# Kernel optimization log

Hardware: AMD Instinct MI355X
Metric: run time of the kernel (lower is better)

## Reference

```python
import jax, jax.numpy as jnp
import numpy as np

N_NODES = 100000
KERNEL_SIZE = 2  # per dim, dim=1 -> 2 kernel weight matrices


def spline_conv(x, edge_index, W, root, bias):
    """PyG SplineConv, dim=1, kernel_size=2, degree=1 open B-spline, aggr='mean'.

    edge_attr is ones (built inside the torch forward), clamped to [0,1].
    Open linear B-spline with K=2: v = u*(K-1); idx = clip(floor(v), 0, K-2) == 0;
    frac = v - idx. Basis weights (1-frac, frac) on kernel indices (0, 1).
    """
    src, dst = edge_index[0], edge_index[1]  # messages flow src -> dst
    E = src.shape[0]
    u = jnp.ones((E,), x.dtype)              # edge pseudo-coordinates (clamped ones)
    v = u * (KERNEL_SIZE - 1)
    idx = jnp.clip(jnp.floor(v), 0, KERNEL_SIZE - 2)  # always 0 for K=2
    frac = v - idx                            # in [0,1]
    # Transform all nodes by both kernel weight matrices once: (2, N, out)
    xw = jnp.einsum('ni,kio->kno', x, W)
    # Per-edge basis-weighted message (idx==0 => kernel indices 0 and 1)
    msg = (1.0 - frac)[:, None] * xw[0, src] + frac[:, None] * xw[1, src]
    agg = jax.ops.segment_sum(msg, dst, num_segments=N_NODES)
    deg = jax.ops.segment_sum(jnp.ones((E,), x.dtype), dst, num_segments=N_NODES)
    agg = agg / jnp.clip(deg, 1.0)[:, None]   # mean aggregation
    return agg + x @ root + bias


def setup_inputs() -> dict:
    key = jax.random.key(0)
    ks = jax.random.split(key, 8)
    N, F, H, C, E = N_NODES, 128, 16, 40, 3200000
    x = jax.random.normal(ks[0], (N, F), dtype=jnp.float32)
    edge_index = jax.random.randint(ks[1], (2, E), 0, N, dtype=jnp.int32)
    W1 = jax.random.normal(ks[2], (2, F, H), dtype=jnp.float32) * 0.1
    root1 = jax.random.normal(ks[3], (F, H), dtype=jnp.float32) * 0.1
    b1 = jnp.zeros((H,), dtype=jnp.float32)
    W2 = jax.random.normal(ks[4], (2, H, C), dtype=jnp.float32) * 0.1
    root2 = jax.random.normal(ks[5], (H, C), dtype=jnp.float32) * 0.1
    b2 = jnp.zeros((C,), dtype=jnp.float32)
    return {"x": x, "edge_index": edge_index, "W1": W1, "root1": root1,
            "b1": b1, "W2": W2, "root2": root2, "b2": b2}


def reference(x, edge_index, W1, root1, b1, W2, root2, b2):
    # eval mode: F.dropout(training=False) is identity
    h = jax.nn.elu(spline_conv(x, edge_index, W1, root1, b1))
    out = spline_conv(h, edge_index, W2, root2, b2)
    return jax.nn.log_softmax(out, axis=1)
```

## Files before the change

### kernel.cpp

```cpp
#include <hip/hip_runtime.h>
#include <hip/hip_bf16.h>

#define N_NODES 100000
#define FIN 128
#define HID 16
#define NCLS 40
#define NEDGE 3200000
#define NBUCK 391
#define NCHUNK 782
#define W_ROW 144

typedef int v4i __attribute__((ext_vector_type(4)));

__device__ __forceinline__ unsigned short f2b(float f) {
  union { float f; unsigned u; } v;
  v.f = f;
  unsigned r = v.u + 0x7FFFu + ((v.u >> 16) & 1u);
  return (unsigned short)(r >> 16);
}

__device__ __forceinline__ void accum8(uint4 w, float* a) {
  union { unsigned u; float f; } t;
  t.u = w.x << 16;         a[0] += t.f;
  t.u = w.x & 0xFFFF0000u; a[1] += t.f;
  t.u = w.y << 16;         a[2] += t.f;
  t.u = w.y & 0xFFFF0000u; a[3] += t.f;
  t.u = w.z << 16;         a[4] += t.f;
  t.u = w.z & 0xFFFF0000u; a[5] += t.f;
  t.u = w.w << 16;         a[6] += t.f;
  t.u = w.w & 0xFFFF0000u; a[7] += t.f;
}

__global__ __launch_bounds__(256) void proj1_kernel(
    const float* __restrict__ x, const float* __restrict__ W1,
    const float* __restrict__ root1,
    unsigned* __restrict__ xw1b, float* __restrict__ xr1) {
  __shared__ float Wl[32 * W_ROW];

  int tid = threadIdx.x;
  for (int t = tid; t < 32 * FIN; t += 256) {
    int c = t >> 7, k = t & 127;
    float v = (c < 16) ? W1[FIN * HID + k * HID + c] : root1[k * HID + (c - 16)];
    Wl[c * W_ROW + k + ((k >> 5) << 2)] = v;
  }
  __syncthreads();

  int n = blockIdx.x * 64 + (tid >> 2);
  int j = tid & 3;
  bool live = (n < N_NODES);

  float4 xv[8];
  if (live) {
    const float4* xr = (const float4*)(x + (size_t)n * FIN + j * 32);
#pragma unroll
    for (int m = 0; m < 8; ++m) xv[m] = xr[m];
  } else {
#pragma unroll
    for (int m = 0; m < 8; ++m) xv[m] = make_float4(0.f, 0.f, 0.f, 0.f);
  }

  float acc[32];
  const float* wj = Wl + j * 36;
#pragma unroll 4
  for (int c = 0; c < 32; ++c) {
    const float4* wr = (const float4*)(wj + c * W_ROW);
    float s = 0.f;
#pragma unroll
    for (int m = 0; m < 8; ++m) {
      float4 wv = wr[m];
      s += xv[m].x * wv.x + xv[m].y * wv.y + xv[m].z * wv.z + xv[m].w * wv.w;
    }
    acc[c] = s;
  }

#pragma unroll
  for (int c = 0; c < 32; ++c) {
    acc[c] += __shfl_xor(acc[c], 1);
    acc[c] += __shfl_xor(acc[c], 2);
  }
  if (!live) return;

  if (j == 0) {
    uint4 pk;
    pk.x = (unsigned)f2b(acc[0]) | ((unsigned)f2b(acc[1]) << 16);
    pk.y = (unsigned)f2b(acc[2]) | ((unsigned)f2b(acc[3]) << 16);
    pk.z = (unsigned)f2b(acc[4]) | ((unsigned)f2b(acc[5]) << 16);
    pk.w = (unsigned)f2b(acc[6]) | ((unsigned)f2b(acc[7]) << 16);
    *(uint4*)((char*)xw1b + (size_t)n * 32) = pk;
  } else if (j == 1) {
    uint4 pk;
    pk.x = (unsigned)f2b(acc[8]) | ((unsigned)f2b(acc[9]) << 16);
    pk.y = (unsigned)f2b(acc[10]) | ((unsigned)f2b(acc[11]) << 16);
    pk.z = (unsigned)f2b(acc[12]) | ((unsigned)f2b(acc[13]) << 16);
    pk.w = (unsigned)f2b(acc[14]) | ((unsigned)f2b(acc[15]) << 16);
    *(uint4*)((char*)xw1b + (size_t)n * 32 + 16) = pk;
  } else if (j == 2) {
    *(float4*)(xr1 + (size_t)n * 16 + 0) =
        make_float4(acc[16], acc[17], acc[18], acc[19]);
    *(float4*)(xr1 + (size_t)n * 16 + 4) =
        make_float4(acc[20], acc[21], acc[22], acc[23]);
  } else {
    *(float4*)(xr1 + (size_t)n * 16 + 8) =
        make_float4(acc[24], acc[25], acc[26], acc[27]);
    *(float4*)(xr1 + (size_t)n * 16 + 12) =
        make_float4(acc[28], acc[29], acc[30], acc[31]);
  }
}

__global__ __launch_bounds__(512) void histB_kernel(
    const int* __restrict__ dst, int* __restrict__ bcnt) {
  __shared__ int hc[NBUCK];
  for (int t = threadIdx.x; t < NBUCK; t += 512) hc[t] = 0;
  __syncthreads();
  int base = blockIdx.x * 4096;
#pragma unroll
  for (int k = 0; k < 8; ++k) {
    int e = base + k * 512 + threadIdx.x;
    if (e < NEDGE) atomicAdd(&hc[dst[e] >> 8], 1);
  }
  __syncthreads();
  for (int t = threadIdx.x; t < NBUCK; t += 512) {
    int v = hc[t];
    if (v) atomicAdd(&bcnt[t], v);
  }
}

__global__ __launch_bounds__(512) void scan_kernel(
    const int* __restrict__ bcnt, int* __restrict__ boff,
    int* __restrict__ gcursor, int* __restrict__ rowptr) {
  __shared__ int s[512];
  int v = (threadIdx.x < NBUCK) ? bcnt[threadIdx.x] : 0;
  s[threadIdx.x] = v;
  __syncthreads();
  for (int off = 1; off < 512; off <<= 1) {
    int t = (threadIdx.x >= off) ? s[threadIdx.x - off] : 0;
    __syncthreads();
    s[threadIdx.x] += t;
    __syncthreads();
  }
  if (threadIdx.x < NBUCK) {
    int e = s[threadIdx.x] - v;
    boff[threadIdx.x] = e;
    gcursor[threadIdx.x] = e;
  }
  if (threadIdx.x == 0) {
    boff[NBUCK] = NEDGE;
    rowptr[N_NODES] = NEDGE;
  }
}

__global__ __launch_bounds__(512) void partA_kernel(
    const int* __restrict__ src, const int* __restrict__ dst,
    int* __restrict__ gcursor, unsigned* __restrict__ recs) {
  __shared__ int cnt[NBUCK];
  __shared__ int base[NBUCK];
  for (int t = threadIdx.x; t < NBUCK; t += 512) cnt[t] = 0;
  __syncthreads();

  int ebase = blockIdx.x * 4096;
  unsigned recv[8];
  int bk[8];
  int rank[8];
#pragma unroll
  for (int k = 0; k < 8; ++k) {
    int e = ebase + k * 512 + threadIdx.x;
    if (e < NEDGE) {
      int d = dst[e];
      bk[k] = d >> 8;
      recv[k] = (unsigned)src[e] | ((unsigned)(d & 255) << 17);
      rank[k] = atomicAdd(&cnt[bk[k]], 1);
    } else {
      bk[k] = -1;
    }
  }
  __syncthreads();
  for (int t = threadIdx.x; t < NBUCK; t += 512) {
    int cv = cnt[t];
    base[t] = cv ? atomicAdd(&gcursor[t], cv) : 0;
  }
  __syncthreads();
#pragma unroll
  for (int k = 0; k < 8; ++k)
    if (bk[k] >= 0) recs[base[bk[k]] + rank[k]] = recv[k];
}

__global__ __launch_bounds__(1024) void sortB_kernel(
    const int* __restrict__ boff, const unsigned* __restrict__ recs,
    int* __restrict__ rowptr, int* __restrict__ colsrc) {
  __shared__ int hist[256];
  __shared__ int s[256];
  __shared__ int cur[256];
  if (threadIdx.x < 256) hist[threadIdx.x] = 0;
  __syncthreads();

  int b = blockIdx.x;
  int beg = boff[b], end = boff[b + 1];
  for (int j = beg + threadIdx.x; j < end; j += 1024)
    atomicAdd(&hist[recs[j] >> 17], 1);
  __syncthreads();

  if (threadIdx.x < 256) s[threadIdx.x] = hist[threadIdx.x];
  __syncthreads();
  for (int off = 1; off < 256; off <<= 1) {
    int t = 0;
    if (threadIdx.x < 256 && threadIdx.x >= off) t = s[threadIdx.x - off];
    __syncthreads();
    if (threadIdx.x < 256) s[threadIdx.x] += t;
    __syncthreads();
  }
  if (threadIdx.x < 256) {
    int excl = s[threadIdx.x] - hist[threadIdx.x];
    int n = b * 256 + threadIdx.x;
    if (n < N_NODES) rowptr[n] = beg + excl;
    cur[threadIdx.x] = excl;
  }
  __syncthreads();

  for (int j = beg + threadIdx.x; j < end; j += 1024) {
    unsigned r = recs[j];
    int dl = r >> 17;
    int pos = atomicAdd(&cur[dl], 1);
    colsrc[beg + pos] = (int)(r & 0x1FFFF);
  }
}

__global__ __launch_bounds__(256) void gather1_kernel(
    const int* __restrict__ rowptr, const int* __restrict__ colsrc,
    const uint4* __restrict__ valb8, const float4* __restrict__ xr14,
    const float* __restrict__ b1, float4* __restrict__ h4,
    uint4* __restrict__ hb8) {
  int t = blockIdx.x * 256 + threadIdx.x;
  int n = t >> 3;
  if (n >= N_NODES) return;
  int d = t & 1;
  int p = (t >> 1) & 3;
  int beg = rowptr[n], end = rowptr[n + 1];

  float a[8] = {0.f, 0.f, 0.f, 0.f, 0.f, 0.f, 0.f, 0.f};
  int bA = (beg + 3) & ~3;
  int eA = end & ~3;
  if (bA > eA) {
    if (p == 0)
      for (int j = beg; j < end; ++j) accum8(valb8[colsrc[j] * 2 + d], a);
  } else {
    if (p == 0) {
      for (int j = beg; j < bA; ++j) accum8(valb8[colsrc[j] * 2 + d], a);
    } else if (p == 3) {
      for (int j = eA; j < end; ++j) accum8(valb8[colsrc[j] * 2 + d], a);
    }
    float a1[8] = {0.f, 0.f, 0.f, 0.f, 0.f, 0.f, 0.f, 0.f};
    int j = bA + p * 4;
    for (; j + 20 <= eA; j += 32) {
      v4i c0 = __builtin_nontemporal_load((const v4i*)(colsrc + j));
      v4i c1 = __builtin_nontemporal_load((const v4i*)(colsrc + j + 16));
      uint4 w0 = valb8[c0.x * 2 + d];
      uint4 w1 = valb8[c0.y * 2 + d];
      uint4 w2 = valb8[c0.z * 2 + d];
      uint4 w3 = valb8[c0.w * 2 + d];
      uint4 w4 = valb8[c1.x * 2 + d];
      uint4 w5 = valb8[c1.y * 2 + d];
      uint4 w6 = valb8[c1.z * 2 + d];
      uint4 w7 = valb8[c1.w * 2 + d];
      accum8(w0, a);
      accum8(w1, a1);
      accum8(w2, a);
      accum8(w3, a1);
      accum8(w4, a);
      accum8(w5, a1);
      accum8(w6, a);
      accum8(w7, a1);
    }
    for (; j + 4 <= eA; j += 16) {
      v4i c0 = __builtin_nontemporal_load((const v4i*)(colsrc + j));
      accum8(valb8[c0.x * 2 + d], a);
      accum8(valb8[c0.y * 2 + d], a1);
      accum8(valb8[c0.z * 2 + d], a);
      accum8(valb8[c0.w * 2 + d], a1);
    }
#pragma unroll
    for (int k = 0; k < 8; ++k) a[k] += a1[k];
  }

#pragma unroll
  for (int k = 0; k < 8; ++k) {
    a[k] += __shfl_xor(a[k], 2);
    a[k] += __shfl_xor(a[k], 4);
  }
  if (p) return;

  float inv = 1.0f / fmaxf((float)(end - beg), 1.0f);
  float4 r0 = xr14[n * 4 + 2 * d];
  float4 r1 = xr14[n * 4 + 2 * d + 1];
  const float4* bb = (const float4*)b1;
  float4 bb0 = bb[2 * d], bb1 = bb[2 * d + 1];
  float o[8];
  o[0] = a[0] * inv + r0.x + bb0.x;
  o[1] = a[1] * inv + r0.y + bb0.y;
  o[2] = a[2] * inv + r0.z + bb0.z;
  o[3] = a[3] * inv + r0.w + bb0.w;
  o[4] = a[4] * inv + r1.x + bb1.x;
  o[5] = a[5] * inv + r1.y + bb1.y;
  o[6] = a[6] * inv + r1.z + bb1.z;
  o[7] = a[7] * inv + r1.w + bb1.w;
#pragma unroll
  for (int k = 0; k < 8; ++k) o[k] = (o[k] > 0.f) ? o[k] : expm1f(o[k]);
  h4[n * 4 + 2 * d] = make_float4(o[0], o[1], o[2], o[3]);
  h4[n * 4 + 2 * d + 1] = make_float4(o[4], o[5], o[6], o[7]);
  uint4 pk;
  pk.x = (unsigned)f2b(o[0]) | ((unsigned)f2b(o[1]) << 16);
  pk.y = (unsigned)f2b(o[2]) | ((unsigned)f2b(o[3]) << 16);
  pk.z = (unsigned)f2b(o[4]) | ((unsigned)f2b(o[5]) << 16);
  pk.w = (unsigned)f2b(o[6]) | ((unsigned)f2b(o[7]) << 16);
  hb8[n * 2 + d] = pk;
}

__global__ __launch_bounds__(256) void gather2_kernel(
    const int* __restrict__ rowptr, const int* __restrict__ colsrc,
    const uint4* __restrict__ valb8, float4* __restrict__ agg2n4) {
  int t = blockIdx.x * 256 + threadIdx.x;
  int n = t >> 3;
  if (n >= N_NODES) return;
  int d = t & 1;
  int p = (t >> 1) & 3;
  int beg = rowptr[n], end = rowptr[n + 1];

  float a[8] = {0.f, 0.f, 0.f, 0.f, 0.f, 0.f, 0.f, 0.f};
  int bA = (beg + 3) & ~3;
  int eA = end & ~3;
  if (bA > eA) {
    if (p == 0)
      for (int j = beg; j < end; ++j) accum8(valb8[colsrc[j] * 2 + d], a);
  } else {
    if (p == 0) {
      for (int j = beg; j < bA; ++j) accum8(valb8[colsrc[j] * 2 + d], a);
    } else if (p == 3) {
      for (int j = eA; j < end; ++j) accum8(valb8[colsrc[j] * 2 + d], a);
    }
    float a1[8] = {0.f, 0.f, 0.f, 0.f, 0.f, 0.f, 0.f, 0.f};
    int j = bA + p * 4;
    for (; j + 20 <= eA; j += 32) {
      v4i c0 = __builtin_nontemporal_load((const v4i*)(colsrc + j));
      v4i c1 = __builtin_nontemporal_load((const v4i*)(colsrc + j + 16));
      uint4 w0 = valb8[c0.x * 2 + d];
      uint4 w1 = valb8[c0.y * 2 + d];
      uint4 w2 = valb8[c0.z * 2 + d];
      uint4 w3 = valb8[c0.w * 2 + d];
      uint4 w4 = valb8[c1.x * 2 + d];
      uint4 w5 = valb8[c1.y * 2 + d];
      uint4 w6 = valb8[c1.z * 2 + d];
      uint4 w7 = valb8[c1.w * 2 + d];
      accum8(w0, a);
      accum8(w1, a1);
      accum8(w2, a);
      accum8(w3, a1);
      accum8(w4, a);
      accum8(w5, a1);
      accum8(w6, a);
      accum8(w7, a1);
    }
    for (; j + 4 <= eA; j += 16) {
      v4i c0 = __builtin_nontemporal_load((const v4i*)(colsrc + j));
      accum8(valb8[c0.x * 2 + d], a);
      accum8(valb8[c0.y * 2 + d], a1);
      accum8(valb8[c0.z * 2 + d], a);
      accum8(valb8[c0.w * 2 + d], a1);
    }
#pragma unroll
    for (int k = 0; k < 8; ++k) a[k] += a1[k];
  }

#pragma unroll
  for (int k = 0; k < 8; ++k) {
    a[k] += __shfl_xor(a[k], 2);
    a[k] += __shfl_xor(a[k], 4);
  }
  if (p) return;

  float inv = 1.0f / fmaxf((float)(end - beg), 1.0f);
  agg2n4[n * 4 + 2 * d] =
      make_float4(a[0] * inv, a[1] * inv, a[2] * inv, a[3] * inv);
  agg2n4[n * 4 + 2 * d + 1] =
      make_float4(a[4] * inv, a[5] * inv, a[6] * inv, a[7] * inv);
}

__global__ __launch_bounds__(256) void out_kernel(
    const float* __restrict__ h, const float* __restrict__ agg2n,
    const float* __restrict__ W2, const float* __restrict__ root2,
    const float* __restrict__ b2v, float* __restrict__ out) {
  __shared__ float Wl[HID * NCLS];
  __shared__ float Rl[HID * NCLS];
  __shared__ float Bl[NCLS];
  for (int i = threadIdx.x; i < HID * NCLS; i += blockDim.x) {
    Wl[i] = W2[HID * NCLS + i];
    Rl[i] = root2[i];
  }
  if (threadIdx.x < NCLS) Bl[threadIdx.x] = b2v[threadIdx.x];
  __syncthreads();

  int n = blockIdx.x * blockDim.x + threadIdx.x;
  if (n >= N_NODES) return;

  float hv[HID], av[HID];
#pragma unroll
  for (int c = 0; c < HID; ++c) {
    hv[c] = h[n * HID + c];
    av[c] = agg2n[n * HID + c];
  }
  float logit[NCLS];
#pragma unroll
  for (int j = 0; j < NCLS; ++j) logit[j] = Bl[j];
  for (int c = 0; c < HID; ++c) {
    float hc = hv[c], ac = av[c];
#pragma unroll
    for (int j = 0; j < NCLS; ++j)
      logit[j] += ac * Wl[c * NCLS + j] + hc * Rl[c * NCLS + j];
  }
  float m = -INFINITY;
#pragma unroll
  for (int j = 0; j < NCLS; ++j) m = fmaxf(m, logit[j]);
  float s = 0.f;
#pragma unroll
  for (int j = 0; j < NCLS; ++j) s += expf(logit[j] - m);
  float lse = m + logf(s);
#pragma unroll
  for (int j = 0; j < NCLS; ++j)
    out[(size_t)n * NCLS + j] = logit[j] - lse;
}

extern "C" void kernel_launch(void* const* d_in, const int* in_sizes, int n_in,
                              void* d_out, int out_size, void* d_ws,
                              size_t ws_size, hipStream_t stream) {
  const float* x = (const float*)d_in[0];
  const int* ei = (const int*)d_in[1];
  const float* W1 = (const float*)d_in[2];
  const float* root1 = (const float*)d_in[3];
  const float* b1 = (const float*)d_in[4];
  const float* W2 = (const float*)d_in[5];
  const float* root2 = (const float*)d_in[6];
  const float* b2v = (const float*)d_in[7];
  float* out = (float*)d_out;

  const int* src = ei;
  const int* dstp = ei + NEDGE;

  char* w = (char*)d_ws;
  int* bcnt = (int*)w;           w += 2048;
  int* boff = (int*)w;           w += 2048;
  int* gcursor = (int*)w;        w += 2048;
  int* rowptr = (int*)w;         w += (size_t)(N_NODES + 4) * 4;
  unsigned* recs = (unsigned*)w; w += (size_t)NEDGE * 4;
  int* colsrc = (int*)w;         w += (size_t)NEDGE * 4;
  unsigned* xw1b = (unsigned*)w; w += (size_t)N_NODES * HID * 2;
  float* xr1 = (float*)w;        w += (size_t)N_NODES * HID * 4;
  unsigned short* hb = (unsigned short*)w; w += (size_t)N_NODES * HID * 2;

  float* h = (float*)recs;
  float* agg2n = (float*)((char*)recs + (size_t)N_NODES * HID * 4);

  hipMemsetAsync(bcnt, 0, 2048, stream);

  proj1_kernel<<<(N_NODES + 63) / 64, 256, 0, stream>>>(x, W1, root1, xw1b,
                                                        xr1);
  histB_kernel<<<NCHUNK, 512, 0, stream>>>(dstp, bcnt);
  scan_kernel<<<1, 512, 0, stream>>>(bcnt, boff, gcursor, rowptr);
  partA_kernel<<<NCHUNK, 512, 0, stream>>>(src, dstp, gcursor, recs);
  sortB_kernel<<<NBUCK, 1024, 0, stream>>>(boff, recs, rowptr, colsrc);
  gather1_kernel<<<(N_NODES * 8 + 255) / 256, 256, 0, stream>>>(
      rowptr, colsrc, (const uint4*)xw1b, (const float4*)xr1, b1, (float4*)h,
      (uint4*)hb);
  gather2_kernel<<<(N_NODES * 8 + 255) / 256, 256, 0, stream>>>(
      rowptr, colsrc, (const uint4*)hb, (float4*)agg2n);
  out_kernel<<<(N_NODES + 255) / 256, 256, 0, stream>>>(h, agg2n, W2, root2,
                                                        b2v, out);
}
```

Before: 291.9 us.

## Vectorize edge loads and stage bucket scatter writes in LDS for coalescing

The histogram and partition kernels now read dst/src with int4 vector loads, eight contiguous edges per thread. The partition kernel also sorts its records by bucket in shared memory through a block-local scan, then writes them out contiguously instead of scattering them. The per-bucket sort kernel stages its output in a 48KB shared buffer and writes colsrc with coalesced stores. The aim is to cut uncoalesced global scatter traffic in CSR construction, at the cost of extra LDS, barriers and lower occupancy.

Result: faster. 273.4 us (-6.3%).

```diff
diff --git a/kernel.cpp b/kernel.cpp
--- a/kernel.cpp
+++ b/kernel.cpp
@@ -9,6 +9,7 @@
 #define NBUCK 391
 #define NCHUNK 782
 #define W_ROW 144
+#define SCAP 12288
 
 typedef int v4i __attribute__((ext_vector_type(4)));
 
@@ -112,11 +113,20 @@
   __shared__ int hc[NBUCK];
   for (int t = threadIdx.x; t < NBUCK; t += 512) hc[t] = 0;
   __syncthreads();
-  int base = blockIdx.x * 4096;
-#pragma unroll
-  for (int k = 0; k < 8; ++k) {
-    int e = base + k * 512 + threadIdx.x;
-    if (e < NEDGE) atomicAdd(&hc[dst[e] >> 8], 1);
+  int e0 = blockIdx.x * 4096 + threadIdx.x * 8;
+  if (e0 + 8 <= NEDGE) {
+    int4 a = *(const int4*)(dst + e0);
+    int4 b = *(const int4*)(dst + e0 + 4);
+    atomicAdd(&hc[a.x >> 8], 1);
+    atomicAdd(&hc[a.y >> 8], 1);
+    atomicAdd(&hc[a.z >> 8], 1);
+    atomicAdd(&hc[a.w >> 8], 1);
+    atomicAdd(&hc[b.x >> 8], 1);
+    atomicAdd(&hc[b.y >> 8], 1);
+    atomicAdd(&hc[b.z >> 8], 1);
+    atomicAdd(&hc[b.w >> 8], 1);
+  } else {
+    for (int e = e0; e < NEDGE; ++e) atomicAdd(&hc[dst[e] >> 8], 1);
   }
   __syncthreads();
   for (int t = threadIdx.x; t < NBUCK; t += 512) {
@@ -153,35 +163,82 @@
     const int* __restrict__ src, const int* __restrict__ dst,
     int* __restrict__ gcursor, unsigned* __restrict__ recs) {
   __shared__ int cnt[NBUCK];
+  __shared__ int start[NBUCK];
   __shared__ int base[NBUCK];
-  for (int t = threadIdx.x; t < NBUCK; t += 512) cnt[t] = 0;
+  __shared__ int scn[512];
+  __shared__ unsigned srec[4096];
+  __shared__ unsigned short sbk[4096];
+
+  int tid = threadIdx.x;
+  for (int t = tid; t < NBUCK; t += 512) cnt[t] = 0;
   __syncthreads();
 
   int ebase = blockIdx.x * 4096;
+  int nblk = NEDGE - ebase;
+  if (nblk > 4096) nblk = 4096;
+
   unsigned recv[8];
   int bk[8];
   int rank[8];
+  int e0 = ebase + tid * 8;
+  if (e0 + 8 <= NEDGE) {
+    int4 d0 = *(const int4*)(dst + e0);
+    int4 d1 = *(const int4*)(dst + e0 + 4);
+    int4 s0 = *(const int4*)(src + e0);
+    int4 s1 = *(const int4*)(src + e0 + 4);
+    int dv[8] = {d0.x, d0.y, d0.z, d0.w, d1.x, d1.y, d1.z, d1.w};
+    int sv[8] = {s0.x, s0.y, s0.z, s0.w, s1.x, s1.y, s1.z, s1.w};
+#pragma unroll
+    for (int k = 0; k < 8; ++k) {
+      bk[k] = dv[k] >> 8;
+      recv[k] = (unsigned)sv[k] | ((unsigned)(dv[k] & 255) << 17);
+      rank[k] = atomicAdd(&cnt[bk[k]], 1);
+    }
+  } else {
+#pragma unroll
+    for (int k = 0; k < 8; ++k) {
+      int e = e0 + k;
+      if (e < NEDGE) {
+        int d = dst[e];
+        bk[k] = d >> 8;
+        recv[k] = (unsigned)src[e] | ((unsigned)(d & 255) << 17);
+        rank[k] = atomicAdd(&cnt[bk[k]], 1);
+      } else {
+        bk[k] = -1;
+      }
+    }
+  }
+  __syncthreads();
+
+  int v = (tid < NBUCK) ? cnt[tid] : 0;
+  scn[tid] = v;
+  __syncthreads();
+  for (int off = 1; off < 512; off <<= 1) {
+    int t = (tid >= off) ? scn[tid - off] : 0;
+    __syncthreads();
+    scn[tid] += t;
+    __syncthreads();
+  }
+  if (tid < NBUCK) {
+    start[tid] = scn[tid] - v;
+    base[tid] = v ? atomicAdd(&gcursor[tid], v) : 0;
+  }
+  __syncthreads();
+
 #pragma unroll
   for (int k = 0; k < 8; ++k) {
-    int e = ebase + k * 512 + threadIdx.x;
-    if (e < NEDGE) {
-      int d = dst[e];
-      bk[k] = d >> 8;
-      recv[k] = (unsigned)src[e] | ((unsigned)(d & 255) << 17);
-      rank[k] = atomicAdd(&cnt[bk[k]], 1);
-    } else {
-      bk[k] = -1;
-    }
-  }
-  __syncthreads();
-  for (int t = threadIdx.x; t < NBUCK; t += 512) {
-    int cv = cnt[t];
-    base[t] = cv ? atomicAdd(&gcursor[t], cv) : 0;
-  }
-  __syncthreads();
-#pragma unroll
-  for (int k = 0; k < 8; ++k)
-    if (bk[k] >= 0) recs[base[bk[k]] + rank[k]] = recv[k];
+    if (bk[k] >= 0) {
+      int pos = start[bk[k]] + rank[k];
+      srec[pos] = recv[k];
+      sbk[pos] = (unsigned short)bk[k];
+    }
+  }
+  __syncthreads();
+
+  for (int i = tid; i < nblk; i += 512) {
+    int b = sbk[i];
+    recs[base[b] + (i - start[b])] = srec[i];
+  }
 }
 
 __global__ __launch_bounds__(1024) void sortB_kernel(
@@ -190,6 +247,7 @@
   __shared__ int hist[256];
   __shared__ int s[256];
   __shared__ int cur[256];
+  __shared__ int staged[SCAP];
   if (threadIdx.x < 256) hist[threadIdx.x] = 0;
   __syncthreads();
 
@@ -220,8 +278,14 @@
     unsigned r = recs[j];
     int dl = r >> 17;
     int pos = atomicAdd(&cur[dl], 1);
-    colsrc[beg + pos] = (int)(r & 0x1FFFF);
-  }
+    if (pos < SCAP) staged[pos] = (int)(r & 0x1FFFF);
+    else colsrc[beg + pos] = (int)(r & 0x1FFFF);
+  }
+  __syncthreads();
+
+  int size = end - beg;
+  if (size > SCAP) size = SCAP;
+  for (int i = threadIdx.x; i < size; i += 1024) colsrc[beg + i] = staged[i];
 }
 
 __global__ __launch_bounds__(256) void gather1_kernel(
```
